# Optimization experiments

Measured on AMD Instinct MI355X. Metric: run time of the kernel, lower is better.

Reference implementation:

```python
import jax, jax.numpy as jnp
import numpy as np

B, H, W, N, DX, DZ = 4, 64, 64, 4096, 2, 128
INIT_LS = 0.1


def setup_inputs() -> dict:
    key = jax.random.key(0)
    k1, k2, k3, k4 = jax.random.split(key, 4)
    xc_off_grid = jax.random.uniform(k1, (B, N, DX), dtype=jnp.float32)
    # regular grid coordinates in [0, 1]^2, broadcast over batch
    gy, gx = jnp.meshgrid(jnp.linspace(0.0, 1.0, H), jnp.linspace(0.0, 1.0, W), indexing="ij")
    xc_on_grid = jnp.broadcast_to(jnp.stack([gy, gx], axis=-1)[None], (B, H, W, DX)).astype(jnp.float32)
    zc_off_grid = jax.random.normal(k2, (B, N, DZ), dtype=jnp.float32)
    zc_on_grid = jax.random.normal(k3, (B, H, W, DZ), dtype=jnp.float32)
    # lengthscale_param = log(exp(init_lengthscale) - 1)  (inverse softplus)
    lengthscale_param = jnp.log(jnp.expm1(jnp.full((DX,), INIT_LS, dtype=jnp.float32)))
    return {
        "xc_off_grid": xc_off_grid,
        "xc_on_grid": xc_on_grid,
        "zc_off_grid": zc_off_grid,
        "zc_on_grid": zc_on_grid,
        "lengthscale_param": lengthscale_param,
        "ignore_on_grid": 0,
    }


def reference(xc_off_grid, xc_on_grid, zc_off_grid, zc_on_grid, lengthscale_param, ignore_on_grid):
    b = xc_on_grid.shape[0]
    grid_shape = xc_on_grid.shape[1:-1]
    dz = zc_off_grid.shape[-1]
    xg = xc_on_grid.reshape(b, -1, xc_on_grid.shape[-1])  # [b, m, dx]
    lengthscale = 1e-05 + jax.nn.softplus(lengthscale_param)  # [dx]
    # squared scaled distances: [b, m, n]
    diff = (xg[:, :, None, :] - xc_off_grid[:, None, :, :]) / lengthscale
    weights = jnp.exp(-0.5 * jnp.sum(diff * diff, axis=-1))  # [b, m, n]
    zc = jnp.einsum("bmn,bnd->bmd", weights, zc_off_grid)  # [b, m, dz]
    if not ignore_on_grid:
        zc = zc + zc_on_grid.reshape(b, -1, dz)
    return zc.reshape((b,) + grid_shape + (dz,))
```

## Files before the change

kernel.cpp:

```cpp
#include <hip/hip_runtime.h>

#define HH 64
#define WW 64
#define NN 4096
#define DZc 128
#define KS 8
#define BK 64
#define NKT (NN / KS / BK)
#define CELLS 2097152
#define WS_NEED (8ull * CELLS * 2ull)

typedef __fp16 v2fp16 __attribute__((ext_vector_type(2)));
typedef _Float16 v4h __attribute__((ext_vector_type(4)));
typedef _Float16 v8h __attribute__((ext_vector_type(8)));
typedef float v16f __attribute__((ext_vector_type(16)));

__device__ __forceinline__ unsigned pk16(float lo, float hi){
  union { v2fp16 h; unsigned u; } c;
  c.h = __builtin_amdgcn_cvt_pkrtz(lo, hi);
  return c.u;
}
__device__ __forceinline__ float fexp2(float x){ return __builtin_amdgcn_exp2f(x); }

__global__ void init_out_kernel(const float4* __restrict__ zc_on,
                                const int* __restrict__ ignore,
                                float4* __restrict__ out){
  int i = blockIdx.x * blockDim.x + threadIdx.x;
  float4 v = zc_on[i];
  if (ignore[0]) { v.x = 0.f; v.y = 0.f; v.z = 0.f; v.w = 0.f; }
  out[i] = v;
}

__global__ void reduce_kernel(const v4h* __restrict__ part,
                              const float4* __restrict__ zc_on,
                              const int* __restrict__ ignore,
                              float4* __restrict__ out){
  int i = blockIdx.x * blockDim.x + threadIdx.x;
  float4 s = zc_on[i];
  if (ignore[0]) { s.x = 0.f; s.y = 0.f; s.z = 0.f; s.w = 0.f; }
  #pragma unroll
  for (int ks = 0; ks < KS; ++ks){
    v4h p = part[(size_t)ks * (CELLS / 4) + i];
    s.x += (float)p[0]; s.y += (float)p[1]; s.z += (float)p[2]; s.w += (float)p[3];
  }
  out[i] = s;
}

__global__ __launch_bounds__(256, 2)
void setconv_gemm_kernel(const float* __restrict__ xc_off,
                         const float* __restrict__ xc_on,
                         const float* __restrict__ zc_off,
                         const float* __restrict__ lsp,
                         _Float16* __restrict__ part,
                         float* __restrict__ out)
{
  __shared__ unsigned short zt[2][128][68];
  __shared__ unsigned short gt[2][40][72];

  const int tid = threadIdx.x;
  const int bid = blockIdx.x;
  const int ks  = bid >> 6;
  const int bm  = bid & 63;
  const int b   = bm >> 4;
  const int mt  = bm & 15;
  const int iy0 = (mt >> 3) * 32;
  const int ix0 = (mt & 7) * 8;
  const int nbase = ks * (NN / KS);

  const float lsy = 1e-5f + log1pf(expf(lsp[0]));
  const float lsx = 1e-5f + log1pf(expf(lsp[1]));
  const float LOG2E = 1.44269504088896340736f;
  const float ay = -0.5f * LOG2E / (lsy * lsy);
  const float ax = -0.5f * LOG2E / (lsx * lsx);

  const int gp = tid & 31;
  const int gr = tid >> 5;
  float gc[5], ga[5];
  #pragma unroll
  for (int i = 0; i < 5; ++i){
    int row = gr + 8 * i;
    if (row < 32){ gc[i] = xc_on[((b * HH + iy0 + row) * WW) * 2];        ga[i] = ay; }
    else         { gc[i] = xc_on[(b * HH * WW + ix0 + row - 32) * 2 + 1]; ga[i] = ax; }
  }

  const int zd  = (tid & 63) | (((tid >> 6) & 1) << 6);
  const int zkh = tid >> 7;

  const int lane = tid & 63;
  const int wv  = tid >> 6;
  const int l31 = lane & 31;
  const int lh  = lane >> 5;
  const int gxr = 32 + (l31 & 7);
  const int gyr = wv * 8 + (l31 >> 3);

  v16f acc[2][4];
  #pragma unroll
  for (int m = 0; m < 2; ++m)
    #pragma unroll
    for (int d = 0; d < 4; ++d)
      #pragma unroll
      for (int r = 0; r < 16; ++r)
        acc[m][d][r] = 0.f;

  const float* xb = xc_off + (size_t)b * NN * 2;
  const float* zb = zc_off + (size_t)b * NN * DZc;

  {
    const int n0 = nbase;
    float4 xq = *(const float4*)&xb[(size_t)(n0 + 2 * gp) * 2];
    unsigned* gw = (unsigned*)&gt[0][0][0];
    #pragma unroll
    for (int i = 0; i < 5; ++i){
      int row = gr + 8 * i;
      float s0 = (row < 32) ? xq.x : xq.y;
      float s1 = (row < 32) ? xq.z : xq.w;
      float d0 = gc[i] - s0, d1 = gc[i] - s1;
      gw[row * 36 + gp] = pk16(fexp2(ga[i] * d0 * d0), fexp2(ga[i] * d1 * d1));
    }
    float zv[32];
    #pragma unroll
    for (int i = 0; i < 32; ++i)
      zv[i] = zb[(size_t)(n0 + zkh * 32 + i) * DZc + zd];
    #pragma unroll
    for (int j = 0; j < 8; ++j){
      union { unsigned u[2]; double d; } w;
      w.u[0] = pk16(zv[4 * j],     zv[4 * j + 1]);
      w.u[1] = pk16(zv[4 * j + 2], zv[4 * j + 3]);
      *(double*)&zt[0][zd][zkh * 32 + 4 * j] = w.d;
    }
  }
  __syncthreads();

  #pragma unroll 1
  for (int kt = 0; kt < NKT; ++kt){
    const int buf  = kt & 1;
    const int nbuf = buf ^ 1;
    const bool have_next = (kt + 1 < NKT);
    const int n1 = nbase + (kt + 1) * BK;

    float zv[32];
    float4 xq_n = (float4){0.f, 0.f, 0.f, 0.f};
    if (have_next){
      #pragma unroll
      for (int i = 0; i < 32; ++i)
        zv[i] = zb[(size_t)(n1 + zkh * 32 + i) * DZc + zd];
      xq_n = *(const float4*)&xb[(size_t)(n1 + 2 * gp) * 2];
    }

    #pragma unroll
    for (int kstep = 0; kstep < 4; ++kstep){
      const int k0 = kstep * 16 + lh * 8;
      const v8h xu = *(const v8h*)&gt[buf][gxr][k0];
      v8h bfr[4];
      #pragma unroll
      for (int dtl = 0; dtl < 4; ++dtl){
        union { v4h h[2]; v8h v; } zu;
        zu.h[0] = *(const v4h*)&zt[buf][dtl * 32 + l31][k0];
        zu.h[1] = *(const v4h*)&zt[buf][dtl * 32 + l31][k0 + 4];
        bfr[dtl] = zu.v;
      }
      #pragma unroll
      for (int mtl = 0; mtl < 2; ++mtl){
        const v8h yu = *(const v8h*)&gt[buf][gyr + mtl * 4][k0];
        v8h av = yu * xu;
        #pragma unroll
        for (int dtl = 0; dtl < 4; ++dtl)
          acc[mtl][dtl] = __builtin_amdgcn_mfma_f32_32x32x16_f16(av, bfr[dtl], acc[mtl][dtl], 0, 0, 0);
      }
    }

    if (have_next){
      #pragma unroll
      for (int j = 0; j < 8; ++j){
        union { unsigned u[2]; double d; } w;
        w.u[0] = pk16(zv[4 * j],     zv[4 * j + 1]);
        w.u[1] = pk16(zv[4 * j + 2], zv[4 * j + 3]);
        *(double*)&zt[nbuf][zd][zkh * 32 + 4 * j] = w.d;
      }
      unsigned* gw = (unsigned*)&gt[nbuf][0][0];
      #pragma unroll
      for (int i = 0; i < 5; ++i){
        int row = gr + 8 * i;
        float s0 = (row < 32) ? xq_n.x : xq_n.y;
        float s1 = (row < 32) ? xq_n.z : xq_n.w;
        float d0 = gc[i] - s0, d1 = gc[i] - s1;
        gw[row * 36 + gp] = pk16(fexp2(ga[i] * d0 * d0), fexp2(ga[i] * d1 * d1));
      }
    }
    __syncthreads();
  }

  if (part){
    _Float16* pw = part + (size_t)ks * CELLS;
    #pragma unroll
    for (int mtl = 0; mtl < 2; ++mtl)
      #pragma unroll
      for (int dtl = 0; dtl < 4; ++dtl){
        const int d = dtl * 32 + l31;
        #pragma unroll
        for (int reg = 0; reg < 16; ++reg){
          const int row = (reg & 3) + 8 * (reg >> 2) + 4 * lh;
          const int m = wv * 64 + mtl * 32 + row;
          const int iy = iy0 + (m >> 3);
          const int ix = ix0 + (m & 7);
          pw[((b * HH + iy) * WW + ix) * DZc + d] = (_Float16)acc[mtl][dtl][reg];
        }
      }
  } else {
    #pragma unroll
    for (int mtl = 0; mtl < 2; ++mtl)
      #pragma unroll
      for (int dtl = 0; dtl < 4; ++dtl){
        const int d = dtl * 32 + l31;
        #pragma unroll
        for (int reg = 0; reg < 16; ++reg){
          const int row = (reg & 3) + 8 * (reg >> 2) + 4 * lh;
          const int m = wv * 64 + mtl * 32 + row;
          const int iy = iy0 + (m >> 3);
          const int ix = ix0 + (m & 7);
          unsafeAtomicAdd(&out[((b * HH + iy) * WW + ix) * DZc + d], acc[mtl][dtl][reg]);
        }
      }
  }
}

extern "C" void kernel_launch(void* const* d_in, const int* in_sizes, int n_in,
                              void* d_out, int out_size, void* d_ws, size_t ws_size,
                              hipStream_t stream){
  const float* xc_off = (const float*)d_in[0];
  const float* xc_on  = (const float*)d_in[1];
  const float* zc_off = (const float*)d_in[2];
  const float* zc_on  = (const float*)d_in[3];
  const float* lsp    = (const float*)d_in[4];
  const int*   ign    = (const int*)d_in[5];
  float* out = (float*)d_out;

  if (ws_size >= WS_NEED){
    _Float16* part = (_Float16*)d_ws;
    setconv_gemm_kernel<<<KS * 64, 256, 0, stream>>>(xc_off, xc_on, zc_off, lsp, part, out);
    reduce_kernel<<<CELLS / 4 / 256, 256, 0, stream>>>((const v4h*)part, (const float4*)zc_on, ign, (float4*)out);
  } else {
    init_out_kernel<<<out_size / 1024, 256, 0, stream>>>((const float4*)zc_on, ign, (float4*)out);
    setconv_gemm_kernel<<<KS * 64, 256, 0, stream>>>(xc_off, xc_on, zc_off, lsp, nullptr, out);
  }
}
```

Before: 108.9 us.

## Halve output tile to 16x8 grid cells and split waves over DZ halves

Shrinks each block's output tile from a 32x8 grid patch to a 16x8 patch and halves the K-tile to 32. The four waves are now arranged as 2 (M) x 2 (DZ halves) instead of 4 along M, which cuts per-thread accumulators from 8 to 4 MFMA tiles. Shared memory per block also shrinks, and launch bounds go up to 4 blocks per CU. The grid doubles to 1024 blocks so more waves are resident to hide global load latency. The cost is that each block re-reads the full z tile for half as much output, which doubles zc_off traffic and the separable-weight exp work per output, and the loop takes more barriers per unit of work.

```diff
diff --git a/kernel.cpp b/kernel.cpp
--- a/kernel.cpp
+++ b/kernel.cpp
@@ -5,7 +5,7 @@
 #define NN 4096
 #define DZc 128
 #define KS 8
-#define BK 64
+#define BK 32
 #define NKT (NN / KS / BK)
 #define CELLS 2097152
 #define WS_NEED (8ull * CELLS * 2ull)
@@ -46,7 +46,7 @@
   out[i] = s;
 }
 
-__global__ __launch_bounds__(256, 2)
+__global__ __launch_bounds__(256, 4)
 void setconv_gemm_kernel(const float* __restrict__ xc_off,
                          const float* __restrict__ xc_on,
                          const float* __restrict__ zc_off,
@@ -54,16 +54,16 @@
                          _Float16* __restrict__ part,
                          float* __restrict__ out)
 {
-  __shared__ unsigned short zt[2][128][68];
-  __shared__ unsigned short gt[2][40][72];
+  __shared__ unsigned short zt[2][128][34];
+  __shared__ unsigned short gt[2][24][48];
 
   const int tid = threadIdx.x;
   const int bid = blockIdx.x;
-  const int ks  = bid >> 6;
-  const int bm  = bid & 63;
-  const int b   = bm >> 4;
-  const int mt  = bm & 15;
-  const int iy0 = (mt >> 3) * 32;
+  const int ks  = bid >> 7;
+  const int rem = bid & 127;
+  const int b   = rem >> 5;
+  const int mt  = rem & 31;
+  const int iy0 = (mt >> 3) * 16;
   const int ix0 = (mt & 7) * 8;
   const int nbase = ks * (NN / KS);
 
@@ -73,31 +73,29 @@
   const float ay = -0.5f * LOG2E / (lsy * lsy);
   const float ax = -0.5f * LOG2E / (lsx * lsx);
 
-  const int gp = tid & 31;
-  const int gr = tid >> 5;
-  float gc[5], ga[5];
-  #pragma unroll
-  for (int i = 0; i < 5; ++i){
-    int row = gr + 8 * i;
-    if (row < 32){ gc[i] = xc_on[((b * HH + iy0 + row) * WW) * 2];        ga[i] = ay; }
-    else         { gc[i] = xc_on[(b * HH * WW + ix0 + row - 32) * 2 + 1]; ga[i] = ax; }
-  }
-
-  const int zd  = (tid & 63) | (((tid >> 6) & 1) << 6);
-  const int zkh = tid >> 7;
+  const int gp = tid & 15;
+  const int grow = tid >> 4;
+  const float gcy = xc_on[((b * HH + iy0 + grow) * WW) * 2];
+  const bool hasx = (tid < 128);
+  const float gcx = hasx ? xc_on[(b * HH * WW + ix0 + grow) * 2 + 1] : 0.f;
+
+  const int zd = tid & 127;
+  const int nh = tid >> 7;
 
   const int lane = tid & 63;
   const int wv  = tid >> 6;
+  const int wm  = wv >> 1;
+  const int wdh = wv & 1;
   const int l31 = lane & 31;
   const int lh  = lane >> 5;
-  const int gxr = 32 + (l31 & 7);
-  const int gyr = wv * 8 + (l31 >> 3);
-
-  v16f acc[2][4];
+  const int gxr = 16 + (l31 & 7);
+  const int gyr = wm * 8 + (l31 >> 3);
+
+  v16f acc[2][2];
   #pragma unroll
   for (int m = 0; m < 2; ++m)
     #pragma unroll
-    for (int d = 0; d < 4; ++d)
+    for (int d = 0; d < 2; ++d)
       #pragma unroll
       for (int r = 0; r < 16; ++r)
         acc[m][d][r] = 0.f;
@@ -108,25 +106,22 @@
   {
     const int n0 = nbase;
     float4 xq = *(const float4*)&xb[(size_t)(n0 + 2 * gp) * 2];
-    unsigned* gw = (unsigned*)&gt[0][0][0];
-    #pragma unroll
-    for (int i = 0; i < 5; ++i){
-      int row = gr + 8 * i;
-      float s0 = (row < 32) ? xq.x : xq.y;
-      float s1 = (row < 32) ? xq.z : xq.w;
-      float d0 = gc[i] - s0, d1 = gc[i] - s1;
-      gw[row * 36 + gp] = pk16(fexp2(ga[i] * d0 * d0), fexp2(ga[i] * d1 * d1));
-    }
-    float zv[32];
-    #pragma unroll
-    for (int i = 0; i < 32; ++i)
-      zv[i] = zb[(size_t)(n0 + zkh * 32 + i) * DZc + zd];
-    #pragma unroll
-    for (int j = 0; j < 8; ++j){
+    float dy0 = gcy - xq.x, dy1 = gcy - xq.z;
+    ((unsigned*)&gt[0][0][0])[grow * 24 + gp] = pk16(fexp2(ay * dy0 * dy0), fexp2(ay * dy1 * dy1));
+    if (hasx){
+      float dx0 = gcx - xq.y, dx1 = gcx - xq.w;
+      ((unsigned*)&gt[0][0][0])[(16 + grow) * 24 + gp] = pk16(fexp2(ax * dx0 * dx0), fexp2(ax * dx1 * dx1));
+    }
+    float zv[16];
+    #pragma unroll
+    for (int i = 0; i < 16; ++i)
+      zv[i] = zb[(size_t)(n0 + nh * 16 + i) * DZc + zd];
+    #pragma unroll
+    for (int j = 0; j < 4; ++j){
       union { unsigned u[2]; double d; } w;
       w.u[0] = pk16(zv[4 * j],     zv[4 * j + 1]);
       w.u[1] = pk16(zv[4 * j + 2], zv[4 * j + 3]);
-      *(double*)&zt[0][zd][zkh * 32 + 4 * j] = w.d;
+      *(double*)&zt[0][zd][nh * 16 + 4 * j] = w.d;
     }
   }
   __syncthreads();
@@ -138,25 +133,25 @@
     const bool have_next = (kt + 1 < NKT);
     const int n1 = nbase + (kt + 1) * BK;
 
-    float zv[32];
+    float zv[16];
     float4 xq_n = (float4){0.f, 0.f, 0.f, 0.f};
     if (have_next){
       #pragma unroll
-      for (int i = 0; i < 32; ++i)
-        zv[i] = zb[(size_t)(n1 + zkh * 32 + i) * DZc + zd];
+      for (int i = 0; i < 16; ++i)
+        zv[i] = zb[(size_t)(n1 + nh * 16 + i) * DZc + zd];
       xq_n = *(const float4*)&xb[(size_t)(n1 + 2 * gp) * 2];
     }
 
     #pragma unroll
-    for (int kstep = 0; kstep < 4; ++kstep){
+    for (int kstep = 0; kstep < 2; ++kstep){
       const int k0 = kstep * 16 + lh * 8;
       const v8h xu = *(const v8h*)&gt[buf][gxr][k0];
-      v8h bfr[4];
-      #pragma unroll
-      for (int dtl = 0; dtl < 4; ++dtl){
+      v8h bfr[2];
+      #pragma unroll
+      for (int dtl = 0; dtl < 2; ++dtl){
         union { v4h h[2]; v8h v; } zu;
-        zu.h[0] = *(const v4h*)&zt[buf][dtl * 32 + l31][k0];
-        zu.h[1] = *(const v4h*)&zt[buf][dtl * 32 + l31][k0 + 4];
+        zu.h[0] = *(const v4h*)&zt[buf][wdh * 64 + dtl * 32 + l31][k0];
+        zu.h[1] = *(const v4h*)&zt[buf][wdh * 64 + dtl * 32 + l31][k0 + 4];
         bfr[dtl] = zu.v;
       }
       #pragma unroll
@@ -164,27 +159,24 @@
         const v8h yu = *(const v8h*)&gt[buf][gyr + mtl * 4][k0];
         v8h av = yu * xu;
         #pragma unroll
-        for (int dtl = 0; dtl < 4; ++dtl)
+        for (int dtl = 0; dtl < 2; ++dtl)
           acc[mtl][dtl] = __builtin_amdgcn_mfma_f32_32x32x16_f16(av, bfr[dtl], acc[mtl][dtl], 0, 0, 0);
       }
     }
 
     if (have_next){
       #pragma unroll
-      for (int j = 0; j < 8; ++j){
+      for (int j = 0; j < 4; ++j){
         union { unsigned u[2]; double d; } w;
         w.u[0] = pk16(zv[4 * j],     zv[4 * j + 1]);
         w.u[1] = pk16(zv[4 * j + 2], zv[4 * j + 3]);
-        *(double*)&zt[nbuf][zd][zkh * 32 + 4 * j] = w.d;
-      }
-      unsigned* gw = (unsigned*)&gt[nbuf][0][0];
-      #pragma unroll
-      for (int i = 0; i < 5; ++i){
-        int row = gr + 8 * i;
-        float s0 = (row < 32) ? xq_n.x : xq_n.y;
-        float s1 = (row < 32) ? xq_n.z : xq_n.w;
-        float d0 = gc[i] - s0, d1 = gc[i] - s1;
-        gw[row * 36 + gp] = pk16(fexp2(ga[i] * d0 * d0), fexp2(ga[i] * d1 * d1));
+        *(double*)&zt[nbuf][zd][nh * 16 + 4 * j] = w.d;
+      }
+      float dy0 = gcy - xq_n.x, dy1 = gcy - xq_n.z;
+      ((unsigned*)&gt[nbuf][0][0])[grow * 24 + gp] = pk16(fexp2(ay * dy0 * dy0), fexp2(ay * dy1 * dy1));
+      if (hasx){
+        float dx0 = gcx - xq_n.y, dx1 = gcx - xq_n.w;
+        ((unsigned*)&gt[nbuf][0][0])[(16 + grow) * 24 + gp] = pk16(fexp2(ax * dx0 * dx0), fexp2(ax * dx1 * dx1));
       }
     }
     __syncthreads();
@@ -195,12 +187,12 @@
     #pragma unroll
     for (int mtl = 0; mtl < 2; ++mtl)
       #pragma unroll
-      for (int dtl = 0; dtl < 4; ++dtl){
-        const int d = dtl * 32 + l31;
+      for (int dtl = 0; dtl < 2; ++dtl){
+        const int d = wdh * 64 + dtl * 32 + l31;
         #pragma unroll
         for (int reg = 0; reg < 16; ++reg){
           const int row = (reg & 3) + 8 * (reg >> 2) + 4 * lh;
-          const int m = wv * 64 + mtl * 32 + row;
+          const int m = wm * 64 + mtl * 32 + row;
           const int iy = iy0 + (m >> 3);
           const int ix = ix0 + (m & 7);
           pw[((b * HH + iy) * WW + ix) * DZc + d] = (_Float16)acc[mtl][dtl][reg];
@@ -210,12 +202,12 @@
     #pragma unroll
     for (int mtl = 0; mtl < 2; ++mtl)
       #pragma unroll
-      for (int dtl = 0; dtl < 4; ++dtl){
-        const int d = dtl * 32 + l31;
+      for (int dtl = 0; dtl < 2; ++dtl){
+        const int d = wdh * 64 + dtl * 32 + l31;
         #pragma unroll
         for (int reg = 0; reg < 16; ++reg){
           const int row = (reg & 3) + 8 * (reg >> 2) + 4 * lh;
-          const int m = wv * 64 + mtl * 32 + row;
+          const int m = wm * 64 + mtl * 32 + row;
           const int iy = iy0 + (m >> 3);
           const int ix = ix0 + (m & 7);
           unsafeAtomicAdd(&out[((b * HH + iy) * WW + ix) * DZc + d], acc[mtl][dtl][reg]);
@@ -237,10 +229,10 @@
 
   if (ws_size >= WS_NEED){
     _Float16* part = (_Float16*)d_ws;
-    setconv_gemm_kernel<<<KS * 64, 256, 0, stream>>>(xc_off, xc_on, zc_off, lsp, part, out);
+    setconv_gemm_kernel<<<KS * 128, 256, 0, stream>>>(xc_off, xc_on, zc_off, lsp, part, out);
     reduce_kernel<<<CELLS / 4 / 256, 256, 0, stream>>>((const v4h*)part, (const float4*)zc_on, ign, (float4*)out);
   } else {
     init_out_kernel<<<out_size / 1024, 256, 0, stream>>>((const float4*)zc_on, ign, (float4*)out);
-    setconv_gemm_kernel<<<KS * 64, 256, 0, stream>>>(xc_off, xc_on, zc_off, lsp, nullptr, out);
-  }
-}
+    setconv_gemm_kernel<<<KS * 128, 256, 0, stream>>>(xc_off, xc_on, zc_off, lsp, nullptr, out);
+  }
+}
```

New measurement: 114.0 us. 4.7% more time.
